# Optimization experiments

Hardware: AMD Instinct MI355X
Metric: run time of the kernel (lower is better)

Reference implementation:

```python
import jax, jax.numpy as jnp
import numpy as np

K = 3  # dynamic filter kernel size
EPS = 1e-10


def _filter_norm_spatial(s, std_param):
    # s: (B, K*K, H, W); normalize over filter-tap dim (unbiased std, as torch)
    s = s - s.mean(axis=1, keepdims=True)
    s = s / (s.std(axis=1, keepdims=True, ddof=1) + EPS)
    return s * std_param[None, :, None, None]


def _filter_norm_channel(cf, std_param, B, C):
    # cf: (B, C*K*K); normalize over the K*K taps of each channel
    cf = cf.reshape(B, C, K * K)
    cf = cf - cf.mean(axis=2, keepdims=True)
    cf = cf / (cf.std(axis=2, keepdims=True, ddof=1) + EPS)
    cf = cf.reshape(B, C * K * K) * std_param[None, :]
    return cf.reshape(B, C, K * K)


def _ddf_pack(x, sw, sb, sstd, cw1, cb1, cw2, cb2, cstd):
    B, C, H, W = x.shape
    # spatial branch: 1x1 conv -> per-pixel K*K spatial filter
    s = jnp.einsum('bchw,oc->bohw', x, sw) + sb[None, :, None, None]
    s = _filter_norm_spatial(s, sstd)                      # (B, 9, H, W)
    # channel branch: GAP -> SE MLP -> per-channel K*K filter
    g = x.mean(axis=(2, 3))                                # (B, C)
    h = jax.nn.relu(g @ cw1.T + cb1)                       # (B, mid)
    cf = h @ cw2.T + cb2                                   # (B, C*9)
    cf = _filter_norm_channel(cf, cstd, B, C)              # (B, C, 9)
    # apply decoupled dynamic filter: w[b,c,uv,h,w] = cf[b,c,uv] * s[b,uv,h,w]
    pad = K // 2
    xp = jnp.pad(x, ((0, 0), (0, 0), (pad, pad), (pad, pad)))
    # patches: (B, C, 9, H, W) -- the 9 shifted views (unfold)
    patches = jnp.stack([xp[:, :, i:i + H, j:j + W]
                         for i in range(K) for j in range(K)], axis=2)
    return jnp.einsum('bckhw,bck,bkhw->bchw', patches, cf, s)


def setup_inputs() -> dict:
    key = jax.random.key(0)
    ks = jax.random.split(key, 20)
    nf, mid = 64, 12
    std_scale = np.sqrt(2.0) / K  # calculate_gain('relu') / kernel_size
    d = {'x': jax.random.normal(ks[0], (4, nf, 256, 256), jnp.float32)}
    i = 1
    for p in ('1', '2'):
        d['sw' + p] = jax.random.normal(ks[i], (K * K, nf), jnp.float32) * 0.1; i += 1
        d['sb' + p] = jax.random.normal(ks[i], (K * K,), jnp.float32) * 0.1; i += 1
        d['sstd' + p] = jax.random.normal(ks[i], (K * K,), jnp.float32) * std_scale; i += 1
        d['cw1_' + p] = jax.random.normal(ks[i], (mid, nf), jnp.float32) * 0.1; i += 1
        d['cb1_' + p] = jax.random.normal(ks[i], (mid,), jnp.float32) * 0.1; i += 1
        d['cw2_' + p] = jax.random.normal(ks[i], (nf * K * K, mid), jnp.float32) * 0.1; i += 1
        d['cb2_' + p] = jax.random.normal(ks[i], (nf * K * K,), jnp.float32) * 0.1; i += 1
        d['cstd' + p] = jax.random.normal(ks[i], (nf * K * K,), jnp.float32) * std_scale; i += 1
    return d


def reference(x, sw1, sb1, sstd1, cw1_1, cb1_1, cw2_1, cb2_1, cstd1,
              sw2, sb2, sstd2, cw1_2, cb1_2, cw2_2, cb2_2, cstd2):
    out = _ddf_pack(x, sw1, sb1, sstd1, cw1_1, cb1_1, cw2_1, cb2_1, cstd1)
    out = jax.nn.relu(out)
    out = _ddf_pack(out, sw2, sb2, sstd2, cw1_2, cb1_2, cw2_2, cb2_2, cstd2)
    return x + out
```

## Files before the change

kernel.cpp:

```cpp
#include <hip/hip_runtime.h>

#define B_ 4
#define C_ 64
#define H_ 256
#define W_ 256
#define HW_ (H_*W_)
#define MID_ 12
#define NPB_ 256

__device__ __forceinline__ float wave_reduce64(float v) {
#pragma unroll
    for (int off = 32; off; off >>= 1) v += __shfl_xor(v, off, 64);
    return v;
}

__device__ __forceinline__ void fnorm9(float* t9, const float* __restrict__ sstd) {
    float mean = 0.f;
#pragma unroll
    for (int t = 0; t < 9; ++t) mean += t9[t];
    mean *= (1.f / 9.f);
    float var = 0.f;
#pragma unroll
    for (int t = 0; t < 9; ++t) { float d = t9[t] - mean; var += d * d; }
    float inv = 1.f / (sqrtf(var * (1.f / 8.f)) + 1e-10f);
#pragma unroll
    for (int t = 0; t < 9; ++t) t9[t] = (t9[t] - mean) * inv * sstd[t];
}

__global__ __launch_bounds__(256) void prep_kernel(const float* __restrict__ x,
    const float* __restrict__ sw, const float* __restrict__ sb,
    const float* __restrict__ sstd, float* __restrict__ sarr, float* __restrict__ gp) {
    const int lane = threadIdx.x & 63, wv = threadIdx.x >> 6;
    const int col = blockIdx.x * 64 + lane;
    const int row = blockIdx.y * 4 + wv;
    const int b = blockIdx.z;
    const int bslot = blockIdx.y * gridDim.x + blockIdx.x;
    const int pix = row * W_ + col;
    __shared__ float lg[4][C_];

    float st[9];
#pragma unroll
    for (int t = 0; t < 9; ++t) st[t] = sb[t];

    const float* xb = x + (size_t)b * C_ * HW_;
    float vA[8], vB[8];
#pragma unroll
    for (int i = 0; i < 8; ++i) vA[i] = xb[(size_t)i * HW_ + pix];

    for (int c8 = 0; c8 < C_; c8 += 16) {
#pragma unroll
        for (int i = 0; i < 8; ++i) vB[i] = xb[(size_t)(c8 + 8 + i) * HW_ + pix];
#pragma unroll
        for (int i = 0; i < 8; ++i) {
#pragma unroll
            for (int t = 0; t < 9; ++t) st[t] = fmaf(vA[i], sw[t * C_ + c8 + i], st[t]);
            float g = wave_reduce64(vA[i]);
            if (lane == 0) lg[wv][c8 + i] = g;
        }
        if (c8 + 16 < C_) {
#pragma unroll
            for (int i = 0; i < 8; ++i) vA[i] = xb[(size_t)(c8 + 16 + i) * HW_ + pix];
        }
#pragma unroll
        for (int i = 0; i < 8; ++i) {
#pragma unroll
            for (int t = 0; t < 9; ++t) st[t] = fmaf(vB[i], sw[t * C_ + c8 + 8 + i], st[t]);
            float g = wave_reduce64(vB[i]);
            if (lane == 0) lg[wv][c8 + 8 + i] = g;
        }
    }
    fnorm9(st, sstd);
    {
        float* sp = sarr + ((size_t)b * 9) * HW_ + pix;
#pragma unroll
        for (int t = 0; t < 9; ++t) sp[(size_t)t * HW_] = st[t];
    }
    __syncthreads();
    if (threadIdx.x < C_) {
        int c = threadIdx.x;
        float s4 = lg[0][c] + lg[1][c] + lg[2][c] + lg[3][c];
        gp[((size_t)b * C_ + c) * NPB_ + bslot] = s4;
    }
}

__global__ __launch_bounds__(256) void cfk(const float* __restrict__ gp,
    const float* __restrict__ cw1, const float* __restrict__ cb1,
    const float* __restrict__ cw2, const float* __restrict__ cb2,
    const float* __restrict__ cstd, float* __restrict__ cf) {
    const int tid = threadIdx.x;
    const int b = tid >> 6, c = tid & 63;
    __shared__ float gsm[B_][C_];
    __shared__ float hsm[B_][MID_];
    {
        const float4* p4 = (const float4*)(gp + ((size_t)b * C_ + c) * NPB_);
        float s = 0.f;
#pragma unroll 4
        for (int i = 0; i < NPB_ / 4; ++i) { float4 v = p4[i]; s += (v.x + v.y) + (v.z + v.w); }
        gsm[b][c] = s * (1.f / HW_);
    }
    __syncthreads();
    if (tid < B_ * MID_) {
        int b2 = tid / MID_, m = tid % MID_;
        float a = cb1[m];
        for (int cc = 0; cc < C_; ++cc) a = fmaf(gsm[b2][cc], cw1[m * C_ + cc], a);
        hsm[b2][m] = fmaxf(a, 0.f);
    }
    __syncthreads();
    float v[9];
    float mean = 0.f;
#pragma unroll
    for (int t = 0; t < 9; ++t) {
        int o = c * 9 + t;
        float a = cb2[o];
#pragma unroll
        for (int m = 0; m < MID_; ++m) a = fmaf(hsm[b][m], cw2[o * MID_ + m], a);
        v[t] = a;
        mean += a;
    }
    mean *= (1.f / 9.f);
    float var = 0.f;
#pragma unroll
    for (int t = 0; t < 9; ++t) { float d = v[t] - mean; var += d * d; }
    float inv = 1.f / (sqrtf(var * (1.f / 8.f)) + 1e-10f);
    float* o12 = cf + ((size_t)b * C_ + c) * 12;
#pragma unroll
    for (int t = 0; t < 9; ++t) o12[t] = (v[t] - mean) * inv * cstd[c * 9 + t];
    o12[9] = 0.f; o12[10] = 0.f; o12[11] = 0.f;
}

template<bool PASS1>
__global__ __launch_bounds__(256) void apply_kernel(const float* __restrict__ in,
    const float* __restrict__ sarr, const float* __restrict__ cf,
    const float* __restrict__ swn, const float* __restrict__ sbn,
    const float* __restrict__ sstdn, const float* __restrict__ resid,
    float* __restrict__ out, float* __restrict__ snext, float* __restrict__ gpn) {
    const int lane = threadIdx.x & 63, wv = threadIdx.x >> 6;
    const int col = blockIdx.x * 64 + lane;
    const int row = blockIdx.y * 4 + wv;
    const int b = blockIdx.z;
    const int bslot = blockIdx.y * gridDim.x + blockIdx.x;
    const int pix = row * W_ + col;
    __shared__ float lg[4][C_];

    float s0m[9];
    int off9[9];
    {
        const float* sp = sarr + ((size_t)b * 9) * HW_ + pix;
#pragma unroll
        for (int t = 0; t < 9; ++t) s0m[t] = sp[(size_t)t * HW_];
#pragma unroll
        for (int dr = -1; dr <= 1; ++dr)
#pragma unroll
            for (int dc = -1; dc <= 1; ++dc) {
                const int t = (dr + 1) * 3 + (dc + 1);
                const bool ok = (row + dr >= 0) && (row + dr < H_) &&
                                (col + dc >= 0) && (col + dc < W_);
                off9[t] = ok ? (pix + dr * W_ + dc) : pix;
                if (!ok) s0m[t] = 0.f;
            }
    }
    float nt[9];
    if (PASS1) {
#pragma unroll
        for (int t = 0; t < 9; ++t) nt[t] = sbn[t];
    }

    const float* inb = in + (size_t)b * C_ * HW_;
    const float* cfb = cf + ((size_t)b * C_) * 12;
    const float* rb  = PASS1 ? nullptr : (resid + (size_t)b * C_ * HW_);
    float* outp = out + (size_t)b * C_ * HW_;

    float mA[9], mB[9], rA = 0.f, rB = 0.f;

#define LOAD9(M, RV, cc) do {                                        \
        const float* cbp_ = inb + (size_t)(cc) * HW_;                \
        _Pragma("unroll")                                            \
        for (int t_ = 0; t_ < 9; ++t_) M[t_] = cbp_[off9[t_]];       \
        if (!PASS1) RV = rb[(size_t)(cc) * HW_ + pix];               \
    } while (0)

#define COMPUTE(M, RV, cc) do {                                      \
        const float* cfc_ = cfb + (size_t)(cc) * 12;                 \
        float acc_ = 0.f;                                            \
        _Pragma("unroll")                                            \
        for (int t_ = 0; t_ < 9; ++t_)                               \
            acc_ = fmaf(M[t_] * s0m[t_], cfc_[t_], acc_);            \
        float o_;                                                    \
        if (PASS1) {                                                 \
            o_ = fmaxf(acc_, 0.f);                                   \
            _Pragma("unroll")                                        \
            for (int t_ = 0; t_ < 9; ++t_)                           \
                nt[t_] = fmaf(o_, swn[t_ * C_ + (cc)], nt[t_]);      \
            float g_ = wave_reduce64(o_);                            \
            if (lane == 0) lg[wv][cc] = g_;                          \
        } else {                                                     \
            o_ = acc_ + RV;                                          \
        }                                                            \
        outp[(size_t)(cc) * HW_ + pix] = o_;                         \
    } while (0)

    LOAD9(mA, rA, 0);
    for (int c = 0; c < C_; c += 2) {
        LOAD9(mB, rB, c + 1);
        COMPUTE(mA, rA, c);
        if (c + 2 < C_) LOAD9(mA, rA, c + 2);
        COMPUTE(mB, rB, c + 1);
    }
#undef LOAD9
#undef COMPUTE

    if (PASS1) {
        fnorm9(nt, sstdn);
        {
            float* sp = snext + ((size_t)b * 9) * HW_ + pix;
#pragma unroll
            for (int t = 0; t < 9; ++t) sp[(size_t)t * HW_] = nt[t];
        }
        __syncthreads();
        if (threadIdx.x < C_) {
            int c = threadIdx.x;
            float s4 = lg[0][c] + lg[1][c] + lg[2][c] + lg[3][c];
            gpn[((size_t)b * C_ + c) * NPB_ + bslot] = s4;
        }
    }
}

extern "C" void kernel_launch(void* const* d_in, const int* in_sizes, int n_in,
                              void* d_out, int out_size, void* d_ws, size_t ws_size,
                              hipStream_t stream) {
    const float* x     = (const float*)d_in[0];
    const float* sw1   = (const float*)d_in[1];
    const float* sb1   = (const float*)d_in[2];
    const float* sstd1 = (const float*)d_in[3];
    const float* cw1_1 = (const float*)d_in[4];
    const float* cb1_1 = (const float*)d_in[5];
    const float* cw2_1 = (const float*)d_in[6];
    const float* cb2_1 = (const float*)d_in[7];
    const float* cstd1 = (const float*)d_in[8];
    const float* sw2   = (const float*)d_in[9];
    const float* sb2   = (const float*)d_in[10];
    const float* sstd2 = (const float*)d_in[11];
    const float* cw1_2 = (const float*)d_in[12];
    const float* cb1_2 = (const float*)d_in[13];
    const float* cw2_2 = (const float*)d_in[14];
    const float* cb2_2 = (const float*)d_in[15];
    const float* cstd2 = (const float*)d_in[16];
    float* outp = (float*)d_out;

    const size_t n_out1 = (size_t)B_ * C_ * HW_;
    const size_t n_s    = (size_t)B_ * 9 * HW_;
    const size_t n_cf   = (size_t)B_ * C_ * 12;
    const size_t n_gp   = (size_t)B_ * C_ * NPB_;
    const size_t need = (n_out1 + 2 * n_s + 2 * n_cf + 2 * n_gp) * sizeof(float);
    if (ws_size < need) return;

    float* out1 = (float*)d_ws;
    float* s1   = out1 + n_out1;
    float* s2   = s1 + n_s;
    float* cf1  = s2 + n_s;
    float* cf2  = cf1 + n_cf;
    float* gp1  = cf2 + n_cf;
    float* gp2  = gp1 + n_gp;

    dim3 g(W_ / 64, H_ / 4, B_);

    prep_kernel<<<g, 256, 0, stream>>>(x, sw1, sb1, sstd1, s1, gp1);
    cfk<<<1, 256, 0, stream>>>(gp1, cw1_1, cb1_1, cw2_1, cb2_1, cstd1, cf1);
    apply_kernel<true><<<g, 256, 0, stream>>>(x, s1, cf1, sw2, sb2, sstd2,
                                              nullptr, out1, s2, gp2);
    cfk<<<1, 256, 0, stream>>>(gp2, cw1_2, cb1_2, cw2_2, cb2_2, cstd2, cf2);
    apply_kernel<false><<<g, 256, 0, stream>>>(out1, s2, cf2, nullptr, nullptr,
                                               nullptr, x, outp, nullptr, nullptr);
}
```

Measured before the change: 151.8 us.

## Stage 3x3 halo tiles in LDS with double-buffered 8-channel chunks

The apply kernel now loads each 8-channel block of input, including a one-pixel halo, into double-buffered shared memory through cooperative coalesced loads. The 3x3 taps then read from LDS instead of issuing nine overlapping global loads per pixel per channel. The grid is flattened to a 1D tile index with a swizzle that reorders tiles across rows, aiming for better cache locality. The change adds LDS traffic, two barriers per chunk and more registers for staging offsets, which may reduce occupancy.

```diff
diff --git a/kernel.cpp b/kernel.cpp
--- a/kernel.cpp
+++ b/kernel.cpp
@@ -134,30 +134,38 @@
     const float* __restrict__ swn, const float* __restrict__ sbn,
     const float* __restrict__ sstdn, const float* __restrict__ resid,
     float* __restrict__ out, float* __restrict__ snext, float* __restrict__ gpn) {
-    const int lane = threadIdx.x & 63, wv = threadIdx.x >> 6;
-    const int col = blockIdx.x * 64 + lane;
-    const int row = blockIdx.y * 4 + wv;
-    const int b = blockIdx.z;
-    const int bslot = blockIdx.y * gridDim.x + blockIdx.x;
+    const int tid = threadIdx.x;
+    const int lane = tid & 63, wv = tid >> 6;
+    const int f = blockIdx.x;
+    const int b = blockIdx.y;
+    const int swz = (f & 7) * 32 + (f >> 3);
+    const int bx = swz & 3, by = swz >> 2;
+    const int col0 = bx * 64, row0 = by * 4;
+    const int col = col0 + lane, row = row0 + wv;
     const int pix = row * W_ + col;
+
+    __shared__ float sm[2][8][6][68];
     __shared__ float lg[4][C_];
 
-    float s0m[9];
-    int off9[9];
+    int goff[13]; float gmask[13]; int loff[13];
+#pragma unroll
+    for (int j = 0; j < 13; ++j) {
+        int i = tid + j * 256;
+        int ch = i / 396; int rem = i - ch * 396;
+        int rr = rem / 66; int cx = rem - rr * 66;
+        int gr = row0 - 1 + rr, gc = col0 - 1 + cx;
+        bool valid = i < 3168;
+        bool ok = valid && (gr >= 0) && (gr < H_) && (gc >= 0) && (gc < W_);
+        goff[j] = ok ? (ch * HW_ + gr * W_ + gc) : 0;
+        gmask[j] = ok ? 1.f : 0.f;
+        loff[j] = valid ? (ch * 408 + rr * 68 + cx) : -1;
+    }
+
+    float s0[9];
     {
         const float* sp = sarr + ((size_t)b * 9) * HW_ + pix;
 #pragma unroll
-        for (int t = 0; t < 9; ++t) s0m[t] = sp[(size_t)t * HW_];
-#pragma unroll
-        for (int dr = -1; dr <= 1; ++dr)
-#pragma unroll
-            for (int dc = -1; dc <= 1; ++dc) {
-                const int t = (dr + 1) * 3 + (dc + 1);
-                const bool ok = (row + dr >= 0) && (row + dr < H_) &&
-                                (col + dc >= 0) && (col + dc < W_);
-                off9[t] = ok ? (pix + dr * W_ + dc) : pix;
-                if (!ok) s0m[t] = 0.f;
-            }
+        for (int t = 0; t < 9; ++t) s0[t] = sp[(size_t)t * HW_];
     }
     float nt[9];
     if (PASS1) {
@@ -170,44 +178,71 @@
     const float* rb  = PASS1 ? nullptr : (resid + (size_t)b * C_ * HW_);
     float* outp = out + (size_t)b * C_ * HW_;
 
-    float mA[9], mB[9], rA = 0.f, rB = 0.f;
-
-#define LOAD9(M, RV, cc) do {                                        \
-        const float* cbp_ = inb + (size_t)(cc) * HW_;                \
-        _Pragma("unroll")                                            \
-        for (int t_ = 0; t_ < 9; ++t_) M[t_] = cbp_[off9[t_]];       \
-        if (!PASS1) RV = rb[(size_t)(cc) * HW_ + pix];               \
+    float rstg[13], rv[8];
+
+#define STAGE_LOAD(CH0) do {                                              \
+        const float* cb_ = inb + (size_t)(CH0) * HW_;                     \
+        _Pragma("unroll")                                                 \
+        for (int j_ = 0; j_ < 13; ++j_) rstg[j_] = cb_[goff[j_]] * gmask[j_]; \
     } while (0)
 
-#define COMPUTE(M, RV, cc) do {                                      \
-        const float* cfc_ = cfb + (size_t)(cc) * 12;                 \
-        float acc_ = 0.f;                                            \
-        _Pragma("unroll")                                            \
-        for (int t_ = 0; t_ < 9; ++t_)                               \
-            acc_ = fmaf(M[t_] * s0m[t_], cfc_[t_], acc_);            \
-        float o_;                                                    \
-        if (PASS1) {                                                 \
-            o_ = fmaxf(acc_, 0.f);                                   \
-            _Pragma("unroll")                                        \
-            for (int t_ = 0; t_ < 9; ++t_)                           \
-                nt[t_] = fmaf(o_, swn[t_ * C_ + (cc)], nt[t_]);      \
-            float g_ = wave_reduce64(o_);                            \
-            if (lane == 0) lg[wv][cc] = g_;                          \
-        } else {                                                     \
-            o_ = acc_ + RV;                                          \
-        }                                                            \
-        outp[(size_t)(cc) * HW_ + pix] = o_;                         \
+#define STAGE_WRITE(BUFI) do {                                            \
+        float* sb_ = &sm[BUFI][0][0][0];                                  \
+        _Pragma("unroll")                                                 \
+        for (int j_ = 0; j_ < 13; ++j_)                                   \
+            if (loff[j_] >= 0) sb_[loff[j_]] = rstg[j_];                  \
     } while (0)
 
-    LOAD9(mA, rA, 0);
-    for (int c = 0; c < C_; c += 2) {
-        LOAD9(mB, rB, c + 1);
-        COMPUTE(mA, rA, c);
-        if (c + 2 < C_) LOAD9(mA, rA, c + 2);
-        COMPUTE(mB, rB, c + 1);
-    }
-#undef LOAD9
-#undef COMPUTE
+#define CHUNK_COMPUTE(BUFI, CH0) do {                                     \
+        _Pragma("unroll")                                                 \
+        for (int c_ = 0; c_ < 8; ++c_) {                                  \
+            const float* cfc_ = cfb + (size_t)((CH0) + c_) * 12;          \
+            float acc_ = 0.f;                                             \
+            _Pragma("unroll")                                             \
+            for (int dr_ = 0; dr_ < 3; ++dr_)                             \
+                _Pragma("unroll")                                         \
+                for (int dc_ = 0; dc_ < 3; ++dc_) {                       \
+                    const int t_ = dr_ * 3 + dc_;                         \
+                    acc_ = fmaf(sm[BUFI][c_][wv + dr_][lane + dc_] * s0[t_], \
+                                cfc_[t_], acc_);                          \
+                }                                                         \
+            float o_;                                                     \
+            if (PASS1) {                                                  \
+                o_ = fmaxf(acc_, 0.f);                                    \
+                _Pragma("unroll")                                         \
+                for (int t_ = 0; t_ < 9; ++t_)                            \
+                    nt[t_] = fmaf(o_, swn[t_ * C_ + (CH0) + c_], nt[t_]); \
+                float g_ = wave_reduce64(o_);                             \
+                if (lane == 0) lg[wv][(CH0) + c_] = g_;                   \
+            } else {                                                      \
+                o_ = acc_ + rv[c_];                                       \
+            }                                                             \
+            outp[(size_t)((CH0) + c_) * HW_ + pix] = o_;                  \
+        }                                                                 \
+    } while (0)
+
+    STAGE_LOAD(0);
+    STAGE_WRITE(0);
+    __syncthreads();
+
+#pragma unroll
+    for (int k = 0; k < 8; ++k) {
+        const int ch0 = k * 8;
+        if (k < 7) STAGE_LOAD(ch0 + 8);
+        if (!PASS1) {
+#pragma unroll
+            for (int c = 0; c < 8; ++c) rv[c] = rb[(size_t)(ch0 + c) * HW_ + pix];
+        }
+        if (k & 1) CHUNK_COMPUTE(1, ch0); else CHUNK_COMPUTE(0, ch0);
+        if (k < 7) {
+            __syncthreads();
+            if (k & 1) STAGE_WRITE(0); else STAGE_WRITE(1);
+            __syncthreads();
+        }
+    }
+#undef STAGE_LOAD
+#undef STAGE_WRITE
+#undef CHUNK_COMPUTE
 
     if (PASS1) {
         fnorm9(nt, sstdn);
@@ -217,10 +252,10 @@
             for (int t = 0; t < 9; ++t) sp[(size_t)t * HW_] = nt[t];
         }
         __syncthreads();
-        if (threadIdx.x < C_) {
-            int c = threadIdx.x;
+        if (tid < C_) {
+            int c = tid;
             float s4 = lg[0][c] + lg[1][c] + lg[2][c] + lg[3][c];
-            gpn[((size_t)b * C_ + c) * NPB_ + bslot] = s4;
+            gpn[((size_t)b * C_ + c) * NPB_ + f] = s4;
         }
     }
 }
@@ -262,13 +297,14 @@
     float* gp1  = cf2 + n_cf;
     float* gp2  = gp1 + n_gp;
 
-    dim3 g(W_ / 64, H_ / 4, B_);
-
-    prep_kernel<<<g, 256, 0, stream>>>(x, sw1, sb1, sstd1, s1, gp1);
+    dim3 gp_(W_ / 64, H_ / 4, B_);
+    dim3 ga(256, B_);
+
+    prep_kernel<<<gp_, 256, 0, stream>>>(x, sw1, sb1, sstd1, s1, gp1);
     cfk<<<1, 256, 0, stream>>>(gp1, cw1_1, cb1_1, cw2_1, cb2_1, cstd1, cf1);
-    apply_kernel<true><<<g, 256, 0, stream>>>(x, s1, cf1, sw2, sb2, sstd2,
-                                              nullptr, out1, s2, gp2);
+    apply_kernel<true><<<ga, 256, 0, stream>>>(x, s1, cf1, sw2, sb2, sstd2,
+                                               nullptr, out1, s2, gp2);
     cfk<<<1, 256, 0, stream>>>(gp2, cw1_2, cb1_2, cw2_2, cb2_2, cstd2, cf2);
-    apply_kernel<false><<<g, 256, 0, stream>>>(out1, s2, cf2, nullptr, nullptr,
-                                               nullptr, x, outp, nullptr, nullptr);
-}
+    apply_kernel<false><<<ga, 256, 0, stream>>>(out1, s2, cf2, nullptr, nullptr,
+                                                nullptr, x, outp, nullptr, nullptr);
+}
```

Measured after the change: 185.0 us. 21.9% more time.

## Split apply kernel over channel groups and unfuse next-pass spatial prep

Applied to the files above, without the earlier changes.

The apply kernel now splits the 64 channels into four groups of 16 across the grid's z dimension, giving four times as many blocks. To make that possible, the fused computation of the next pass's spatial filter and global-pool partials is removed from pass 1, and prep_kernel is launched again on out1 instead. This raises parallelism and drops the per-channel wave reductions and shared-memory work from the apply loop. In exchange, out1 (64 MB) has to be read one more time, the spatial filters are reloaded once per channel group, and there is one extra launch. The cfk reduction unroll also goes from 4 to 8.

```diff
diff --git a/kernel.cpp b/kernel.cpp
--- a/kernel.cpp
+++ b/kernel.cpp
@@ -94,7 +94,7 @@
     {
         const float4* p4 = (const float4*)(gp + ((size_t)b * C_ + c) * NPB_);
         float s = 0.f;
-#pragma unroll 4
+#pragma unroll 8
         for (int i = 0; i < NPB_ / 4; ++i) { float4 v = p4[i]; s += (v.x + v.y) + (v.z + v.w); }
         gsm[b][c] = s * (1.f / HW_);
     }
@@ -128,26 +128,24 @@
     o12[9] = 0.f; o12[10] = 0.f; o12[11] = 0.f;
 }
 
-template<bool PASS1>
+template<bool RELU, bool RESID>
 __global__ __launch_bounds__(256) void apply_kernel(const float* __restrict__ in,
     const float* __restrict__ sarr, const float* __restrict__ cf,
-    const float* __restrict__ swn, const float* __restrict__ sbn,
-    const float* __restrict__ sstdn, const float* __restrict__ resid,
-    float* __restrict__ out, float* __restrict__ snext, float* __restrict__ gpn) {
+    const float* __restrict__ resid, float* __restrict__ out) {
     const int lane = threadIdx.x & 63, wv = threadIdx.x >> 6;
     const int col = blockIdx.x * 64 + lane;
     const int row = blockIdx.y * 4 + wv;
-    const int b = blockIdx.z;
-    const int bslot = blockIdx.y * gridDim.x + blockIdx.x;
+    const int z = blockIdx.z;
+    const int b = z >> 2;
+    const int c0 = (z & 3) * 16;
     const int pix = row * W_ + col;
-    __shared__ float lg[4][C_];
-
-    float s0m[9];
+
+    float s0[9];
     int off9[9];
     {
         const float* sp = sarr + ((size_t)b * 9) * HW_ + pix;
 #pragma unroll
-        for (int t = 0; t < 9; ++t) s0m[t] = sp[(size_t)t * HW_];
+        for (int t = 0; t < 9; ++t) s0[t] = sp[(size_t)t * HW_];
 #pragma unroll
         for (int dr = -1; dr <= 1; ++dr)
 #pragma unroll
@@ -156,73 +154,45 @@
                 const bool ok = (row + dr >= 0) && (row + dr < H_) &&
                                 (col + dc >= 0) && (col + dc < W_);
                 off9[t] = ok ? (pix + dr * W_ + dc) : pix;
-                if (!ok) s0m[t] = 0.f;
+                if (!ok) s0[t] = 0.f;
             }
     }
-    float nt[9];
-    if (PASS1) {
-#pragma unroll
-        for (int t = 0; t < 9; ++t) nt[t] = sbn[t];
-    }
-
-    const float* inb = in + (size_t)b * C_ * HW_;
-    const float* cfb = cf + ((size_t)b * C_) * 12;
-    const float* rb  = PASS1 ? nullptr : (resid + (size_t)b * C_ * HW_);
-    float* outp = out + (size_t)b * C_ * HW_;
-
-    float mA[9], mB[9], rA = 0.f, rB = 0.f;
-
-#define LOAD9(M, RV, cc) do {                                        \
-        const float* cbp_ = inb + (size_t)(cc) * HW_;                \
-        _Pragma("unroll")                                            \
-        for (int t_ = 0; t_ < 9; ++t_) M[t_] = cbp_[off9[t_]];       \
-        if (!PASS1) RV = rb[(size_t)(cc) * HW_ + pix];               \
+
+    const float* inb = in + ((size_t)b * C_ + c0) * HW_;
+    const float* cfb = cf + ((size_t)b * C_ + c0) * 12;
+    const float* rb  = RESID ? (resid + ((size_t)b * C_ + c0) * HW_ + pix) : nullptr;
+    float* outp = out + ((size_t)b * C_ + c0) * HW_ + pix;
+
+    float mA[9], mB[9], rAv = 0.f, rBv = 0.f;
+
+#define LD9(M, RV, cc) do {                                                  \
+        const float* p_ = inb + (size_t)(cc) * HW_;                          \
+        _Pragma("unroll")                                                    \
+        for (int t_ = 0; t_ < 9; ++t_) M[t_] = p_[off9[t_]];                 \
+        if (RESID) RV = rb[(size_t)(cc) * HW_];                              \
     } while (0)
 
-#define COMPUTE(M, RV, cc) do {                                      \
-        const float* cfc_ = cfb + (size_t)(cc) * 12;                 \
-        float acc_ = 0.f;                                            \
-        _Pragma("unroll")                                            \
-        for (int t_ = 0; t_ < 9; ++t_)                               \
-            acc_ = fmaf(M[t_] * s0m[t_], cfc_[t_], acc_);            \
-        float o_;                                                    \
-        if (PASS1) {                                                 \
-            o_ = fmaxf(acc_, 0.f);                                   \
-            _Pragma("unroll")                                        \
-            for (int t_ = 0; t_ < 9; ++t_)                           \
-                nt[t_] = fmaf(o_, swn[t_ * C_ + (cc)], nt[t_]);      \
-            float g_ = wave_reduce64(o_);                            \
-            if (lane == 0) lg[wv][cc] = g_;                          \
-        } else {                                                     \
-            o_ = acc_ + RV;                                          \
-        }                                                            \
-        outp[(size_t)(cc) * HW_ + pix] = o_;                         \
+#define CP9(M, RV, cc) do {                                                  \
+        const float* cfc_ = cfb + (size_t)(cc) * 12;                         \
+        float acc_ = 0.f;                                                    \
+        _Pragma("unroll")                                                    \
+        for (int t_ = 0; t_ < 9; ++t_)                                       \
+            acc_ = fmaf(M[t_] * s0[t_], cfc_[t_], acc_);                     \
+        float o_ = RELU ? fmaxf(acc_, 0.f) : acc_;                           \
+        if (RESID) o_ += RV;                                                 \
+        outp[(size_t)(cc) * HW_] = o_;                                       \
     } while (0)
 
-    LOAD9(mA, rA, 0);
-    for (int c = 0; c < C_; c += 2) {
-        LOAD9(mB, rB, c + 1);
-        COMPUTE(mA, rA, c);
-        if (c + 2 < C_) LOAD9(mA, rA, c + 2);
-        COMPUTE(mB, rB, c + 1);
-    }
-#undef LOAD9
-#undef COMPUTE
-
-    if (PASS1) {
-        fnorm9(nt, sstdn);
-        {
-            float* sp = snext + ((size_t)b * 9) * HW_ + pix;
-#pragma unroll
-            for (int t = 0; t < 9; ++t) sp[(size_t)t * HW_] = nt[t];
-        }
-        __syncthreads();
-        if (threadIdx.x < C_) {
-            int c = threadIdx.x;
-            float s4 = lg[0][c] + lg[1][c] + lg[2][c] + lg[3][c];
-            gpn[((size_t)b * C_ + c) * NPB_ + bslot] = s4;
-        }
-    }
+    LD9(mA, rAv, 0);
+#pragma unroll
+    for (int c = 0; c < 16; c += 2) {
+        LD9(mB, rBv, c + 1);
+        CP9(mA, rAv, c);
+        if (c + 2 < 16) LD9(mA, rAv, c + 2);
+        CP9(mB, rBv, c + 1);
+    }
+#undef LD9
+#undef CP9
 }
 
 extern "C" void kernel_launch(void* const* d_in, const int* in_sizes, int n_in,
@@ -262,13 +232,13 @@
     float* gp1  = cf2 + n_cf;
     float* gp2  = gp1 + n_gp;
 
-    dim3 g(W_ / 64, H_ / 4, B_);
-
-    prep_kernel<<<g, 256, 0, stream>>>(x, sw1, sb1, sstd1, s1, gp1);
+    dim3 gprep(W_ / 64, H_ / 4, B_);
+    dim3 gapply(W_ / 64, H_ / 4, B_ * 4);
+
+    prep_kernel<<<gprep, 256, 0, stream>>>(x, sw1, sb1, sstd1, s1, gp1);
     cfk<<<1, 256, 0, stream>>>(gp1, cw1_1, cb1_1, cw2_1, cb2_1, cstd1, cf1);
-    apply_kernel<true><<<g, 256, 0, stream>>>(x, s1, cf1, sw2, sb2, sstd2,
-                                              nullptr, out1, s2, gp2);
+    apply_kernel<true, false><<<gapply, 256, 0, stream>>>(x, s1, cf1, nullptr, out1);
+    prep_kernel<<<gprep, 256, 0, stream>>>(out1, sw2, sb2, sstd2, s2, gp2);
     cfk<<<1, 256, 0, stream>>>(gp2, cw1_2, cb1_2, cw2_2, cb2_2, cstd2, cf2);
-    apply_kernel<false><<<g, 256, 0, stream>>>(out1, s2, cf2, nullptr, nullptr,
-                                               nullptr, x, outp, nullptr, nullptr);
-}
+    apply_kernel<false, true><<<gapply, 256, 0, stream>>>(out1, s2, cf2, x, outp);
+}
```

Result: slower. 167.7 us (+10.5%).
